# Performance work log

Measured on AMD Instinct MI355X. Metric: run time of the kernel, lower is better.

## Reference

```python
import jax, jax.numpy as jnp
import numpy as np

N_USERS = 200000
N_ITEMS = 100000
N_EDGES = 1000000
D = 64
NUM_LAYERS = 3
BATCH = 8192


def setup_inputs() -> dict:
    key = jax.random.key(0)
    ks = jax.random.split(key, 8)
    return {
        "user_feat": jax.random.normal(ks[0], (N_USERS, D), dtype=jnp.float32) * 0.1,
        "item_feat": jax.random.normal(ks[1], (N_ITEMS, D), dtype=jnp.float32) * 0.1,
        "edge_u": jax.random.randint(ks[2], (N_EDGES,), 0, N_USERS, dtype=jnp.int32),
        "edge_i": jax.random.randint(ks[3], (N_EDGES,), 0, N_ITEMS, dtype=jnp.int32),
        "norm": jax.random.uniform(ks[4], (N_EDGES,), dtype=jnp.float32),
        "users": jax.random.randint(ks[5], (BATCH,), 0, N_USERS, dtype=jnp.int32),
        "pos_items": jax.random.randint(ks[6], (BATCH,), 0, N_ITEMS, dtype=jnp.int32),
        "neg_items": jax.random.randint(ks[7], (BATCH,), 0, N_ITEMS, dtype=jnp.int32),
    }


def reference(user_feat, item_feat, edge_u, edge_i, norm, users, pos_items, neg_items):
    # LightGCN propagation: each layer does edge-weighted gather-scatter
    # (u_mul_e 'h','norm' -> sum) in both directions of the bipartite graph.
    u_h, i_h = user_feat, item_feat
    u_acc, i_acc = u_h, i_h
    w = norm[:, None]  # [E, 1]
    for _ in range(NUM_LAYERS):
        # user -> item messages
        new_i = jax.ops.segment_sum(u_h[edge_u] * w, edge_i, num_segments=N_ITEMS)
        # item -> user messages
        new_u = jax.ops.segment_sum(i_h[edge_i] * w, edge_u, num_segments=N_USERS)
        u_h, i_h = new_u, new_i
        u_acc = u_acc + u_h
        i_acc = i_acc + i_h
    scale = 1.0 / (NUM_LAYERS + 1)
    u_acc = u_acc * scale
    i_acc = i_acc * scale
    return (u_acc[users], i_acc[pos_items], i_acc[neg_items])
```

## Files before the change

### kernel.cpp

```cpp
#include <hip/hip_runtime.h>


#define N_USERS 200000
#define N_ITEMS 100000
#define N_EDGES 1000000
#define DIM 64
#define BATCH 8192
#define NTOT (N_USERS + N_ITEMS)
#define NOUT (3 * BATCH)
#define NPART 293
#define PLOCAL 1024
#define CAP 11264

#define HA 489
#define NUNITS (NTOT * DIM / 8)
#define OB (NOUT * 8 / 256)
#define AB8 (NTOT / 32)
#define PRB (NOUT / 1024)
#define PHB (NOUT * 8 / 1024)
#define CVB ((NUNITS + 4095) / 4096)
#define CPB ((NTOT / 4 + 1023) / 1024)

__device__ __forceinline__ unsigned f2bf(float f) {
    unsigned u = __float_as_uint(f);
    return (u + 0x7fffu + ((u >> 16) & 1u)) >> 16;
}
__device__ __forceinline__ uint2 pack4(float4 v) {
    uint2 o;
    o.x = f2bf(v.x) | (f2bf(v.y) << 16);
    o.y = f2bf(v.z) | (f2bf(v.w) << 16);
    return o;
}
__device__ __forceinline__ void fma4(float4& a, uint2 v, float w) {
    a.x += __uint_as_float(v.x << 16) * w;
    a.y += __uint_as_float(v.x & 0xffff0000u) * w;
    a.z += __uint_as_float(v.y << 16) * w;
    a.w += __uint_as_float(v.y & 0xffff0000u) * w;
}
__device__ __forceinline__ int out_bucket(int orow, const int* users,
                                          const int* pos, const int* neg) {
    int seg = orow >> 13;
    int b = orow & (BATCH - 1);
    if (seg == 0) return users[b];
    if (seg == 1) return N_USERS + pos[b];
    return N_USERS + neg[b];
}

__global__ void __launch_bounds__(1024)
prep_kernel(const int* __restrict__ users,
            const int* __restrict__ pos,
            const int* __restrict__ neg,
            const float* __restrict__ u_feat,
            const float* __restrict__ i_feat,
            unsigned char* __restrict__ isOut,
            int* __restrict__ flags,
            float* __restrict__ out)
{
    int bid = blockIdx.x, t = threadIdx.x;
    if (bid < PRB) {
        int orow = bid * 1024 + t;
        int bucket = out_bucket(orow, users, pos, neg);
        isOut[bucket] = 1;
        flags[bucket] = 1;
    } else {
        int idx = (bid - PRB) * 1024 + t;
        int row = idx >> 3;
        int d8 = (idx & 7) << 3;
        int seg = row >> 13;
        int b = row & (BATCH - 1);
        const float* src;
        if (seg == 0)      src = u_feat + (size_t)users[b] * DIM;
        else if (seg == 1) src = i_feat + (size_t)pos[b]   * DIM;
        else               src = i_feat + (size_t)neg[b]   * DIM;
        float4 v0 = *reinterpret_cast<const float4*>(src + d8);
        float4 v1 = *reinterpret_cast<const float4*>(src + d8 + 4);
        v0.x *= 0.25f; v0.y *= 0.25f; v0.z *= 0.25f; v0.w *= 0.25f;
        v1.x *= 0.25f; v1.y *= 0.25f; v1.z *= 0.25f; v1.w *= 0.25f;
        float* op = out + (size_t)row * DIM + d8;
        *reinterpret_cast<float4*>(op) = v0;
        *reinterpret_cast<float4*>(op + 4) = v1;
    }
}

__global__ void scatter_kernel(const int* __restrict__ eu,
                               const int* __restrict__ ei,
                               const float* __restrict__ w,
                               int* __restrict__ gcur,
                               uint2* __restrict__ partBuf,
                               const unsigned char* __restrict__ isOut,
                               int* __restrict__ flags)
{
    __shared__ int lh[NPART];
    __shared__ int lcur[NPART];
    int bid = blockIdx.x, t = threadIdx.x;
    for (int k = t; k < NPART; k += 256) lh[k] = 0;
    __syncthreads();
    int e0 = (bid * 256 + t) * 8;
    bool act = e0 < N_EDGES;
    int4 u0, u1, i0, i1;
    if (act) {
        u0 = *reinterpret_cast<const int4*>(eu + e0);
        u1 = *reinterpret_cast<const int4*>(eu + e0 + 4);
        i0 = *reinterpret_cast<const int4*>(ei + e0);
        i1 = *reinterpret_cast<const int4*>(ei + e0 + 4);
        atomicAdd(&lh[u0.x >> 10], 1);
        atomicAdd(&lh[u0.y >> 10], 1);
        atomicAdd(&lh[u0.z >> 10], 1);
        atomicAdd(&lh[u0.w >> 10], 1);
        atomicAdd(&lh[u1.x >> 10], 1);
        atomicAdd(&lh[u1.y >> 10], 1);
        atomicAdd(&lh[u1.z >> 10], 1);
        atomicAdd(&lh[u1.w >> 10], 1);
        atomicAdd(&lh[(N_USERS + i0.x) >> 10], 1);
        atomicAdd(&lh[(N_USERS + i0.y) >> 10], 1);
        atomicAdd(&lh[(N_USERS + i0.z) >> 10], 1);
        atomicAdd(&lh[(N_USERS + i0.w) >> 10], 1);
        atomicAdd(&lh[(N_USERS + i1.x) >> 10], 1);
        atomicAdd(&lh[(N_USERS + i1.y) >> 10], 1);
        atomicAdd(&lh[(N_USERS + i1.z) >> 10], 1);
        atomicAdd(&lh[(N_USERS + i1.w) >> 10], 1);
    }
    __syncthreads();
    for (int k = t; k < NPART; k += 256) {
        int v = lh[k];
        lcur[k] = v ? atomicAdd(&gcur[k], v) : 0;
    }
    __syncthreads();
    if (act) {
        float4 wa = *reinterpret_cast<const float4*>(w + e0);
        float4 wb = *reinterpret_cast<const float4*>(w + e0 + 4);
        int us[8] = {u0.x, u0.y, u0.z, u0.w, u1.x, u1.y, u1.z, u1.w};
        int is[8] = {i0.x, i0.y, i0.z, i0.w, i1.x, i1.y, i1.z, i1.w};
        float ws[8] = {wa.x, wa.y, wa.z, wa.w, wb.x, wb.y, wb.z, wb.w};
        #pragma unroll
        for (int j = 0; j < 8; ++j) {
            int bu = us[j];
            int bi = N_USERS + is[j];
            unsigned wbits = __float_as_uint(ws[j]);
            int pu = bu >> 10, pi = bi >> 10;
            int su = atomicAdd(&lcur[pu], 1);
            partBuf[(size_t)pu * CAP + su] =
                make_uint2((unsigned)(bu & 1023) | ((unsigned)bi << 10), wbits);
            int si = atomicAdd(&lcur[pi], 1);
            partBuf[(size_t)pi * CAP + si] =
                make_uint2((unsigned)(bi & 1023) | ((unsigned)bu << 10), wbits);
            if (isOut[bu]) flags[bi] = 1;
            if (isOut[bi]) flags[bu] = 1;
        }
    }
}

__global__ void __launch_bounds__(1024)
mid_kernel(const int* __restrict__ gcur,
           const uint2* __restrict__ partBuf,
           int2* __restrict__ rp2,
           int2* __restrict__ entries,
           const float4* __restrict__ uf4,
           const float4* __restrict__ if4,
           unsigned short* __restrict__ F0,
           const int* __restrict__ flags,
           int* __restrict__ list,
           int* __restrict__ count)
{
    __shared__ int h[PLOCAL];
    __shared__ int s[PLOCAL];
    __shared__ int cur[PLOCAL];
    int bid = blockIdx.x, t = threadIdx.x;
    if (bid < NPART) {
        int p = bid;
        int base = p * CAP;
        int end = base + gcur[p];
        h[t] = 0;
        __syncthreads();
        for (int r = base + t; r < end; r += 1024)
            atomicAdd(&h[partBuf[r].x & 1023], 1);
        __syncthreads();
        s[t] = h[t];
        __syncthreads();
        for (int off = 1; off < 1024; off <<= 1) {
            int x = (t >= off) ? s[t - off] : 0;
            __syncthreads();
            s[t] += x;
            __syncthreads();
        }
        int c0 = base + s[t] - h[t];
        cur[t] = c0;
        int gb = p * PLOCAL + t;
        if (gb < NTOT) rp2[gb] = make_int2(c0, h[t]);
        __syncthreads();
        for (int r = base + t; r < end; r += 1024) {
            uint2 rec = partBuf[r];
            int slot = atomicAdd(&cur[rec.x & 1023], 1);
            entries[slot] = make_int2((int)(rec.x >> 10), (int)rec.y);
        }
    } else if (bid < NPART + CVB) {
        const int NU4 = N_USERS * DIM / 4;
        int jb = (bid - NPART) * 4096 + t;
        float4 a[4], b[4];
        #pragma unroll
        for (int c = 0; c < 4; ++c) {
            int j = jb + c * 1024;
            if (j < NUNITS) {
                int f4 = j * 2;
                if (f4 < NU4) { a[c] = uf4[f4];       b[c] = uf4[f4 + 1]; }
                else          { a[c] = if4[f4 - NU4]; b[c] = if4[f4 - NU4 + 1]; }
            }
        }
        #pragma unroll
        for (int c = 0; c < 4; ++c) {
            int j = jb + c * 1024;
            if (j < NUNITS) {
                uint2 pa = pack4(a[c]), pb = pack4(b[c]);
                *reinterpret_cast<uint4*>(F0 + (size_t)j * 8) =
                    make_uint4(pa.x, pa.y, pb.x, pb.y);
            }
        }
    } else {
        int idx = ((bid - NPART - CVB) * 1024 + t) * 4;
        if (idx >= NTOT) return;
        int4 f = *reinterpret_cast<const int4*>(flags + idx);
        int loc[4]; int k = 0;
        if (f.x) loc[k++] = idx;
        if (f.y) loc[k++] = idx + 1;
        if (f.z) loc[k++] = idx + 2;
        if (f.w) loc[k++] = idx + 3;
        if (k) {
            int base = atomicAdd(count, k);
            for (int m = 0; m < k; ++m) list[base + m] = loc[m];
        }
    }
}

__device__ __forceinline__ void agg_row8(int2 rc, int l8, int gb,
                                         const int2* __restrict__ entries,
                                         const unsigned short* __restrict__ src,
                                         float4& sL, float4& sH)
{
    int beg = rc.x, cnt = rc.y;
    float4 a0L = {0,0,0,0}, a0H = {0,0,0,0}, a1L = {0,0,0,0}, a1H = {0,0,0,0};
    for (int base = 0; base < cnt; base += 8) {
        int2 e = make_int2(0, 0);
        if (base + l8 < cnt) e = entries[beg + base + l8];
        int   c[8];
        float wv[8];
        #pragma unroll
        for (int k = 0; k < 8; ++k) {
            c[k]  = __shfl(e.x, gb + k);
            wv[k] = __int_as_float(__shfl(e.y, gb + k));
        }
        uint4 v[8];
        #pragma unroll
        for (int k = 0; k < 8; ++k)
            v[k] = *reinterpret_cast<const uint4*>(
                src + (size_t)c[k] * DIM + l8 * 8);
        #pragma unroll
        for (int k = 0; k < 8; ++k) {
            if (k & 1) {
                fma4(a1L, make_uint2(v[k].x, v[k].y), wv[k]);
                fma4(a1H, make_uint2(v[k].z, v[k].w), wv[k]);
            } else {
                fma4(a0L, make_uint2(v[k].x, v[k].y), wv[k]);
                fma4(a0H, make_uint2(v[k].z, v[k].w), wv[k]);
            }
        }
    }
    sL.x = a0L.x + a1L.x; sL.y = a0L.y + a1L.y;
    sL.z = a0L.z + a1L.z; sL.w = a0L.w + a1L.w;
    sH.x = a0H.x + a1H.x; sH.y = a0H.y + a1H.y;
    sH.z = a0H.z + a1H.z; sH.w = a0H.w + a1H.w;
}

__global__ void agg1_kernel(const int2* __restrict__ rp2,
                            const int2* __restrict__ entries,
                            const unsigned short* __restrict__ F0,
                            unsigned short* __restrict__ H1)
{
    int gid = blockIdx.x * 256 + threadIdx.x;
    int lane = gid & 63;
    int l8 = lane & 7;
    int gb = lane & 56;
    int row = gid >> 3;
    if (row >= NTOT) return;
    float4 sL, sH;
    agg_row8(rp2[row], l8, gb, entries, F0, sL, sH);
    uint2 pL = pack4(sL), pH = pack4(sH);
    *reinterpret_cast<uint4*>(H1 + (size_t)row * DIM + l8 * 8) =
        make_uint4(pL.x, pL.y, pH.x, pH.y);
}

__global__ void agg2_add1_kernel(const int2* __restrict__ rp2,
                                 const int2* __restrict__ entries,
                                 const unsigned short* __restrict__ H1,
                                 unsigned short* __restrict__ H2,
                                 const int* __restrict__ list,
                                 const int* __restrict__ count,
                                 const int* __restrict__ users,
                                 const int* __restrict__ pos,
                                 const int* __restrict__ neg,
                                 float* __restrict__ out)
{
    int bid = blockIdx.x;
    if (bid < AB8) {
        int gid = bid * 256 + threadIdx.x;
        int lane = gid & 63;
        int l8 = lane & 7;
        int gb = lane & 56;
        int idx = gid >> 3;
        int n = *count;
        if (idx >= n) return;
        int row = list[idx];
        float4 sL, sH;
        agg_row8(rp2[row], l8, gb, entries, H1, sL, sH);
        uint2 pL = pack4(sL), pH = pack4(sH);
        *reinterpret_cast<uint4*>(H2 + (size_t)row * DIM + l8 * 8) =
            make_uint4(pL.x, pL.y, pH.x, pH.y);
    } else {
        int idx = (bid - AB8) * 256 + threadIdx.x;
        int row = idx >> 3;
        if (row >= NOUT) return;
        int d8 = (idx & 7) << 3;
        int bucket = out_bucket(row, users, pos, neg);
        uint4 v = *reinterpret_cast<const uint4*>(H1 + (size_t)bucket * DIM + d8);
        float* op = out + (size_t)row * DIM + d8;
        float4 o0 = *reinterpret_cast<const float4*>(op);
        float4 o1 = *reinterpret_cast<const float4*>(op + 4);
        o0.x += 0.25f * __uint_as_float(v.x << 16);
        o0.y += 0.25f * __uint_as_float(v.x & 0xffff0000u);
        o0.z += 0.25f * __uint_as_float(v.y << 16);
        o0.w += 0.25f * __uint_as_float(v.y & 0xffff0000u);
        o1.x += 0.25f * __uint_as_float(v.z << 16);
        o1.y += 0.25f * __uint_as_float(v.z & 0xffff0000u);
        o1.z += 0.25f * __uint_as_float(v.w << 16);
        o1.w += 0.25f * __uint_as_float(v.w & 0xffff0000u);
        *reinterpret_cast<float4*>(op) = o0;
        *reinterpret_cast<float4*>(op + 4) = o1;
    }
}

__global__ void aggout_add2_kernel(const int2* __restrict__ rp2,
                                   const int2* __restrict__ entries,
                                   const unsigned short* __restrict__ H2,
                                   const int* __restrict__ users,
                                   const int* __restrict__ pos,
                                   const int* __restrict__ neg,
                                   float* __restrict__ out)
{
    int gid = blockIdx.x * 256 + threadIdx.x;
    int lane = gid & 63;
    int l8 = lane & 7;
    int gb = lane & 56;
    int orow = gid >> 3;
    if (orow >= NOUT) return;
    int bucket = out_bucket(orow, users, pos, neg);
    float4 sL, sH;
    agg_row8(rp2[bucket], l8, gb, entries, H2, sL, sH);
    uint4 v = *reinterpret_cast<const uint4*>(H2 + (size_t)bucket * DIM + l8 * 8);
    sL.x += __uint_as_float(v.x << 16);
    sL.y += __uint_as_float(v.x & 0xffff0000u);
    sL.z += __uint_as_float(v.y << 16);
    sL.w += __uint_as_float(v.y & 0xffff0000u);
    sH.x += __uint_as_float(v.z << 16);
    sH.y += __uint_as_float(v.z & 0xffff0000u);
    sH.z += __uint_as_float(v.w << 16);
    sH.w += __uint_as_float(v.w & 0xffff0000u);
    float* op = out + (size_t)orow * DIM + l8 * 8;
    float4 o0 = *reinterpret_cast<const float4*>(op);
    float4 o1 = *reinterpret_cast<const float4*>(op + 4);
    o0.x += 0.25f * sL.x; o0.y += 0.25f * sL.y;
    o0.z += 0.25f * sL.z; o0.w += 0.25f * sL.w;
    o1.x += 0.25f * sH.x; o1.y += 0.25f * sH.y;
    o1.z += 0.25f * sH.z; o1.w += 0.25f * sH.w;
    *reinterpret_cast<float4*>(op) = o0;
    *reinterpret_cast<float4*>(op + 4) = o1;
}

extern "C" void kernel_launch(void* const* d_in, const int* in_sizes, int n_in,
                              void* d_out, int out_size, void* d_ws, size_t ws_size,
                              hipStream_t stream)
{
    const float* user_feat = (const float*)d_in[0];
    const float* item_feat = (const float*)d_in[1];
    const int*   eu        = (const int*)d_in[2];
    const int*   ei        = (const int*)d_in[3];
    const float* norm      = (const float*)d_in[4];
    const int*   users     = (const int*)d_in[5];
    const int*   pos       = (const int*)d_in[6];
    const int*   neg       = (const int*)d_in[7];
    float* out = (float*)d_out;

    auto align256 = [](size_t x) { return (x + 255) & ~(size_t)255; };
    const size_t hBytes = (size_t)NTOT * DIM * sizeof(unsigned short);
    const size_t pBytes = (size_t)NPART * CAP * 8;

    char* p = (char*)d_ws;
    unsigned short* F0 = (unsigned short*)p; p += align256(hBytes);
    unsigned short* H1 = (unsigned short*)p; p += align256(hBytes);
    unsigned short* H2 = (unsigned short*)p; p += align256(hBytes);
    const size_t zBytes = (size_t)(512 + NTOT + 16) * 4 + NTOT;
    int* gcur = (int*)p;
    int* flags = gcur + 512;
    int* count = flags + NTOT;
    unsigned char* isOut = (unsigned char*)(count + 16);
    p += align256(zBytes);
    int2* rp2      = (int2*)p;  p += align256((size_t)NTOT * 8);
    uint2* partBuf = (uint2*)p; p += align256(pBytes);
    int*  list     = (int*)p;   p += align256((size_t)NTOT * 4);
    int2* entries  = (int2*)p;  p += align256(pBytes);

    hipMemsetAsync(gcur, 0, zBytes, stream);

    prep_kernel<<<PRB + PHB, 1024, 0, stream>>>(
        users, pos, neg, user_feat, item_feat, isOut, flags, out);

    scatter_kernel<<<HA, 256, 0, stream>>>(
        eu, ei, norm, gcur, partBuf, isOut, flags);

    mid_kernel<<<NPART + CVB + CPB, 1024, 0, stream>>>(
        gcur, partBuf, rp2, entries,
        (const float4*)user_feat, (const float4*)item_feat, F0,
        flags, list, count);

    agg1_kernel<<<AB8, 256, 0, stream>>>(rp2, entries, F0, H1);

    agg2_add1_kernel<<<AB8 + OB, 256, 0, stream>>>(
        rp2, entries, H1, H2, list, count, users, pos, neg, out);

    aggout_add2_kernel<<<NOUT / 32, 256, 0, stream>>>(
        rp2, entries, H2, users, pos, neg, out);
}
```

Before: 267.2 us.

## Co-schedule bf16 conversion with edge scatter; shrink CSR build blocks to 256

```diff
diff --git a/kernel.cpp b/kernel.cpp
--- a/kernel.cpp
+++ b/kernel.cpp
@@ -14,12 +14,12 @@
 
 #define HA 489
 #define NUNITS (NTOT * DIM / 8)
+#define CB ((NUNITS + 1023) / 1024)
 #define OB (NOUT * 8 / 256)
 #define AB8 (NTOT / 32)
 #define PRB (NOUT / 1024)
 #define PHB (NOUT * 8 / 1024)
-#define CVB ((NUNITS + 4095) / 4096)
-#define CPB ((NTOT / 4 + 1023) / 1024)
+#define CPB ((NTOT / 4 + 255) / 256)
 
 __device__ __forceinline__ unsigned f2bf(float f) {
     unsigned u = __float_as_uint(f);
@@ -82,124 +82,84 @@
     }
 }
 
-__global__ void scatter_kernel(const int* __restrict__ eu,
-                               const int* __restrict__ ei,
-                               const float* __restrict__ w,
-                               int* __restrict__ gcur,
-                               uint2* __restrict__ partBuf,
-                               const unsigned char* __restrict__ isOut,
-                               int* __restrict__ flags)
-{
-    __shared__ int lh[NPART];
-    __shared__ int lcur[NPART];
+__global__ void __launch_bounds__(256)
+front_kernel(const int* __restrict__ eu,
+             const int* __restrict__ ei,
+             const float* __restrict__ w,
+             int* __restrict__ gcur,
+             uint2* __restrict__ partBuf,
+             const unsigned char* __restrict__ isOut,
+             int* __restrict__ flags,
+             const float4* __restrict__ uf4,
+             const float4* __restrict__ if4,
+             unsigned short* __restrict__ F0)
+{
     int bid = blockIdx.x, t = threadIdx.x;
-    for (int k = t; k < NPART; k += 256) lh[k] = 0;
-    __syncthreads();
-    int e0 = (bid * 256 + t) * 8;
-    bool act = e0 < N_EDGES;
-    int4 u0, u1, i0, i1;
-    if (act) {
-        u0 = *reinterpret_cast<const int4*>(eu + e0);
-        u1 = *reinterpret_cast<const int4*>(eu + e0 + 4);
-        i0 = *reinterpret_cast<const int4*>(ei + e0);
-        i1 = *reinterpret_cast<const int4*>(ei + e0 + 4);
-        atomicAdd(&lh[u0.x >> 10], 1);
-        atomicAdd(&lh[u0.y >> 10], 1);
-        atomicAdd(&lh[u0.z >> 10], 1);
-        atomicAdd(&lh[u0.w >> 10], 1);
-        atomicAdd(&lh[u1.x >> 10], 1);
-        atomicAdd(&lh[u1.y >> 10], 1);
-        atomicAdd(&lh[u1.z >> 10], 1);
-        atomicAdd(&lh[u1.w >> 10], 1);
-        atomicAdd(&lh[(N_USERS + i0.x) >> 10], 1);
-        atomicAdd(&lh[(N_USERS + i0.y) >> 10], 1);
-        atomicAdd(&lh[(N_USERS + i0.z) >> 10], 1);
-        atomicAdd(&lh[(N_USERS + i0.w) >> 10], 1);
-        atomicAdd(&lh[(N_USERS + i1.x) >> 10], 1);
-        atomicAdd(&lh[(N_USERS + i1.y) >> 10], 1);
-        atomicAdd(&lh[(N_USERS + i1.z) >> 10], 1);
-        atomicAdd(&lh[(N_USERS + i1.w) >> 10], 1);
-    }
-    __syncthreads();
-    for (int k = t; k < NPART; k += 256) {
-        int v = lh[k];
-        lcur[k] = v ? atomicAdd(&gcur[k], v) : 0;
-    }
-    __syncthreads();
-    if (act) {
-        float4 wa = *reinterpret_cast<const float4*>(w + e0);
-        float4 wb = *reinterpret_cast<const float4*>(w + e0 + 4);
-        int us[8] = {u0.x, u0.y, u0.z, u0.w, u1.x, u1.y, u1.z, u1.w};
-        int is[8] = {i0.x, i0.y, i0.z, i0.w, i1.x, i1.y, i1.z, i1.w};
-        float ws[8] = {wa.x, wa.y, wa.z, wa.w, wb.x, wb.y, wb.z, wb.w};
-        #pragma unroll
-        for (int j = 0; j < 8; ++j) {
-            int bu = us[j];
-            int bi = N_USERS + is[j];
-            unsigned wbits = __float_as_uint(ws[j]);
-            int pu = bu >> 10, pi = bi >> 10;
-            int su = atomicAdd(&lcur[pu], 1);
-            partBuf[(size_t)pu * CAP + su] =
-                make_uint2((unsigned)(bu & 1023) | ((unsigned)bi << 10), wbits);
-            int si = atomicAdd(&lcur[pi], 1);
-            partBuf[(size_t)pi * CAP + si] =
-                make_uint2((unsigned)(bi & 1023) | ((unsigned)bu << 10), wbits);
-            if (isOut[bu]) flags[bi] = 1;
-            if (isOut[bi]) flags[bu] = 1;
-        }
-    }
-}
-
-__global__ void __launch_bounds__(1024)
-mid_kernel(const int* __restrict__ gcur,
-           const uint2* __restrict__ partBuf,
-           int2* __restrict__ rp2,
-           int2* __restrict__ entries,
-           const float4* __restrict__ uf4,
-           const float4* __restrict__ if4,
-           unsigned short* __restrict__ F0,
-           const int* __restrict__ flags,
-           int* __restrict__ list,
-           int* __restrict__ count)
-{
-    __shared__ int h[PLOCAL];
-    __shared__ int s[PLOCAL];
-    __shared__ int cur[PLOCAL];
-    int bid = blockIdx.x, t = threadIdx.x;
-    if (bid < NPART) {
-        int p = bid;
-        int base = p * CAP;
-        int end = base + gcur[p];
-        h[t] = 0;
-        __syncthreads();
-        for (int r = base + t; r < end; r += 1024)
-            atomicAdd(&h[partBuf[r].x & 1023], 1);
-        __syncthreads();
-        s[t] = h[t];
-        __syncthreads();
-        for (int off = 1; off < 1024; off <<= 1) {
-            int x = (t >= off) ? s[t - off] : 0;
-            __syncthreads();
-            s[t] += x;
-            __syncthreads();
-        }
-        int c0 = base + s[t] - h[t];
-        cur[t] = c0;
-        int gb = p * PLOCAL + t;
-        if (gb < NTOT) rp2[gb] = make_int2(c0, h[t]);
-        __syncthreads();
-        for (int r = base + t; r < end; r += 1024) {
-            uint2 rec = partBuf[r];
-            int slot = atomicAdd(&cur[rec.x & 1023], 1);
-            entries[slot] = make_int2((int)(rec.x >> 10), (int)rec.y);
-        }
-    } else if (bid < NPART + CVB) {
+    if (bid < HA) {
+        __shared__ int lh[NPART];
+        __shared__ int lcur[NPART];
+        for (int k = t; k < NPART; k += 256) lh[k] = 0;
+        __syncthreads();
+        int e0 = (bid * 256 + t) * 8;
+        bool act = e0 < N_EDGES;
+        int4 u0, u1, i0, i1;
+        if (act) {
+            u0 = *reinterpret_cast<const int4*>(eu + e0);
+            u1 = *reinterpret_cast<const int4*>(eu + e0 + 4);
+            i0 = *reinterpret_cast<const int4*>(ei + e0);
+            i1 = *reinterpret_cast<const int4*>(ei + e0 + 4);
+            atomicAdd(&lh[u0.x >> 10], 1);
+            atomicAdd(&lh[u0.y >> 10], 1);
+            atomicAdd(&lh[u0.z >> 10], 1);
+            atomicAdd(&lh[u0.w >> 10], 1);
+            atomicAdd(&lh[u1.x >> 10], 1);
+            atomicAdd(&lh[u1.y >> 10], 1);
+            atomicAdd(&lh[u1.z >> 10], 1);
+            atomicAdd(&lh[u1.w >> 10], 1);
+            atomicAdd(&lh[(N_USERS + i0.x) >> 10], 1);
+            atomicAdd(&lh[(N_USERS + i0.y) >> 10], 1);
+            atomicAdd(&lh[(N_USERS + i0.z) >> 10], 1);
+            atomicAdd(&lh[(N_USERS + i0.w) >> 10], 1);
+            atomicAdd(&lh[(N_USERS + i1.x) >> 10], 1);
+            atomicAdd(&lh[(N_USERS + i1.y) >> 10], 1);
+            atomicAdd(&lh[(N_USERS + i1.z) >> 10], 1);
+            atomicAdd(&lh[(N_USERS + i1.w) >> 10], 1);
+        }
+        __syncthreads();
+        for (int k = t; k < NPART; k += 256) {
+            int v = lh[k];
+            lcur[k] = v ? atomicAdd(&gcur[k], v) : 0;
+        }
+        __syncthreads();
+        if (act) {
+            float4 wa = *reinterpret_cast<const float4*>(w + e0);
+            float4 wb = *reinterpret_cast<const float4*>(w + e0 + 4);
+            int us[8] = {u0.x, u0.y, u0.z, u0.w, u1.x, u1.y, u1.z, u1.w};
+            int is[8] = {i0.x, i0.y, i0.z, i0.w, i1.x, i1.y, i1.z, i1.w};
+            float ws[8] = {wa.x, wa.y, wa.z, wa.w, wb.x, wb.y, wb.z, wb.w};
+            #pragma unroll
+            for (int j = 0; j < 8; ++j) {
+                int bu = us[j];
+                int bi = N_USERS + is[j];
+                unsigned wbits = __float_as_uint(ws[j]);
+                int pu = bu >> 10, pi = bi >> 10;
+                int su = atomicAdd(&lcur[pu], 1);
+                partBuf[(size_t)pu * CAP + su] =
+                    make_uint2((unsigned)(bu & 1023) | ((unsigned)bi << 10), wbits);
+                int si = atomicAdd(&lcur[pi], 1);
+                partBuf[(size_t)pi * CAP + si] =
+                    make_uint2((unsigned)(bi & 1023) | ((unsigned)bu << 10), wbits);
+                if (isOut[bu]) flags[bi] = 1;
+                if (isOut[bi]) flags[bu] = 1;
+            }
+        }
+    } else {
         const int NU4 = N_USERS * DIM / 4;
-        int jb = (bid - NPART) * 4096 + t;
+        int jb = (bid - HA) * 1024 + t;
         float4 a[4], b[4];
         #pragma unroll
         for (int c = 0; c < 4; ++c) {
-            int j = jb + c * 1024;
+            int j = jb + c * 256;
             if (j < NUNITS) {
                 int f4 = j * 2;
                 if (f4 < NU4) { a[c] = uf4[f4];       b[c] = uf4[f4 + 1]; }
@@ -208,15 +168,65 @@
         }
         #pragma unroll
         for (int c = 0; c < 4; ++c) {
-            int j = jb + c * 1024;
+            int j = jb + c * 256;
             if (j < NUNITS) {
                 uint2 pa = pack4(a[c]), pb = pack4(b[c]);
                 *reinterpret_cast<uint4*>(F0 + (size_t)j * 8) =
                     make_uint4(pa.x, pa.y, pb.x, pb.y);
             }
         }
+    }
+}
+
+__global__ void __launch_bounds__(256)
+csr_compact_kernel(const int* __restrict__ gcur,
+                   const uint2* __restrict__ partBuf,
+                   int2* __restrict__ rp2,
+                   int2* __restrict__ entries,
+                   const int* __restrict__ flags,
+                   int* __restrict__ list,
+                   int* __restrict__ count)
+{
+    int bid = blockIdx.x, t = threadIdx.x;
+    if (bid < NPART) {
+        __shared__ int h[PLOCAL];
+        __shared__ int s[256];
+        __shared__ int cur[PLOCAL];
+        int p = bid;
+        int base = p * CAP;
+        int end = base + gcur[p];
+        h[t * 4 + 0] = 0; h[t * 4 + 1] = 0; h[t * 4 + 2] = 0; h[t * 4 + 3] = 0;
+        __syncthreads();
+        for (int r = base + t; r < end; r += 256)
+            atomicAdd(&h[partBuf[r].x & 1023], 1);
+        __syncthreads();
+        int h0 = h[t * 4], h1 = h[t * 4 + 1], h2 = h[t * 4 + 2], h3 = h[t * 4 + 3];
+        s[t] = h0 + h1 + h2 + h3;
+        __syncthreads();
+        for (int off = 1; off < 256; off <<= 1) {
+            int x = (t >= off) ? s[t - off] : 0;
+            __syncthreads();
+            s[t] += x;
+            __syncthreads();
+        }
+        int b0 = base + ((t == 0) ? 0 : s[t - 1]);
+        cur[t * 4 + 0] = b0;
+        cur[t * 4 + 1] = b0 + h0;
+        cur[t * 4 + 2] = b0 + h0 + h1;
+        cur[t * 4 + 3] = b0 + h0 + h1 + h2;
+        int hv[4] = {h0, h1, h2, h3};
+        int gb = p * PLOCAL + t * 4;
+        #pragma unroll
+        for (int k = 0; k < 4; ++k)
+            if (gb + k < NTOT) rp2[gb + k] = make_int2(cur[t * 4 + k], hv[k]);
+        __syncthreads();
+        for (int r = base + t; r < end; r += 256) {
+            uint2 rec = partBuf[r];
+            int slot = atomicAdd(&cur[rec.x & 1023], 1);
+            entries[slot] = make_int2((int)(rec.x >> 10), (int)rec.y);
+        }
     } else {
-        int idx = ((bid - NPART - CVB) * 1024 + t) * 4;
+        int idx = ((bid - NPART) * 256 + t) * 4;
         if (idx >= NTOT) return;
         int4 f = *reinterpret_cast<const int4*>(flags + idx);
         int loc[4]; int k = 0;
@@ -412,13 +422,12 @@
     prep_kernel<<<PRB + PHB, 1024, 0, stream>>>(
         users, pos, neg, user_feat, item_feat, isOut, flags, out);
 
-    scatter_kernel<<<HA, 256, 0, stream>>>(
-        eu, ei, norm, gcur, partBuf, isOut, flags);
-
-    mid_kernel<<<NPART + CVB + CPB, 1024, 0, stream>>>(
-        gcur, partBuf, rp2, entries,
-        (const float4*)user_feat, (const float4*)item_feat, F0,
-        flags, list, count);
+    front_kernel<<<HA + CB, 256, 0, stream>>>(
+        eu, ei, norm, gcur, partBuf, isOut, flags,
+        (const float4*)user_feat, (const float4*)item_feat, F0);
+
+    csr_compact_kernel<<<NPART + CPB, 256, 0, stream>>>(
+        gcur, partBuf, rp2, entries, flags, list, count);
 
     agg1_kernel<<<AB8, 256, 0, stream>>>(rp2, entries, F0, H1);
 
```

Result: slower. 293.0 us (+9.7%).

## Move bf16 feature conversion into scatter kernel and use nontemporal accesses

Applied to the files above, without the earlier changes.

```diff
diff --git a/kernel.cpp b/kernel.cpp
--- a/kernel.cpp
+++ b/kernel.cpp
@@ -14,12 +14,15 @@
 
 #define HA 489
 #define NUNITS (NTOT * DIM / 8)
+#define CB ((NUNITS + 1023) / 1024)
 #define OB (NOUT * 8 / 256)
 #define AB8 (NTOT / 32)
 #define PRB (NOUT / 1024)
 #define PHB (NOUT * 8 / 1024)
-#define CVB ((NUNITS + 4095) / 4096)
 #define CPB ((NTOT / 4 + 1023) / 1024)
+
+typedef float    floatx4 __attribute__((ext_vector_type(4)));
+typedef unsigned uint4v  __attribute__((ext_vector_type(4)));
 
 __device__ __forceinline__ unsigned f2bf(float f) {
     unsigned u = __float_as_uint(f);
@@ -29,6 +32,12 @@
     uint2 o;
     o.x = f2bf(v.x) | (f2bf(v.y) << 16);
     o.y = f2bf(v.z) | (f2bf(v.w) << 16);
+    return o;
+}
+__device__ __forceinline__ uint2 pack4v(floatx4 v) {
+    uint2 o;
+    o.x = f2bf(v[0]) | (f2bf(v[1]) << 16);
+    o.y = f2bf(v[2]) | (f2bf(v[3]) << 16);
     return o;
 }
 __device__ __forceinline__ void fma4(float4& a, uint2 v, float w) {
@@ -82,91 +91,121 @@
     }
 }
 
-__global__ void scatter_kernel(const int* __restrict__ eu,
-                               const int* __restrict__ ei,
-                               const float* __restrict__ w,
-                               int* __restrict__ gcur,
-                               uint2* __restrict__ partBuf,
-                               const unsigned char* __restrict__ isOut,
-                               int* __restrict__ flags)
-{
-    __shared__ int lh[NPART];
-    __shared__ int lcur[NPART];
+__global__ void __launch_bounds__(256)
+front_kernel(const int* __restrict__ eu,
+             const int* __restrict__ ei,
+             const float* __restrict__ w,
+             int* __restrict__ gcur,
+             uint2* __restrict__ partBuf,
+             const unsigned char* __restrict__ isOut,
+             int* __restrict__ flags,
+             const floatx4* __restrict__ uf4,
+             const floatx4* __restrict__ if4,
+             unsigned short* __restrict__ F0)
+{
     int bid = blockIdx.x, t = threadIdx.x;
-    for (int k = t; k < NPART; k += 256) lh[k] = 0;
-    __syncthreads();
-    int e0 = (bid * 256 + t) * 8;
-    bool act = e0 < N_EDGES;
-    int4 u0, u1, i0, i1;
-    if (act) {
-        u0 = *reinterpret_cast<const int4*>(eu + e0);
-        u1 = *reinterpret_cast<const int4*>(eu + e0 + 4);
-        i0 = *reinterpret_cast<const int4*>(ei + e0);
-        i1 = *reinterpret_cast<const int4*>(ei + e0 + 4);
-        atomicAdd(&lh[u0.x >> 10], 1);
-        atomicAdd(&lh[u0.y >> 10], 1);
-        atomicAdd(&lh[u0.z >> 10], 1);
-        atomicAdd(&lh[u0.w >> 10], 1);
-        atomicAdd(&lh[u1.x >> 10], 1);
-        atomicAdd(&lh[u1.y >> 10], 1);
-        atomicAdd(&lh[u1.z >> 10], 1);
-        atomicAdd(&lh[u1.w >> 10], 1);
-        atomicAdd(&lh[(N_USERS + i0.x) >> 10], 1);
-        atomicAdd(&lh[(N_USERS + i0.y) >> 10], 1);
-        atomicAdd(&lh[(N_USERS + i0.z) >> 10], 1);
-        atomicAdd(&lh[(N_USERS + i0.w) >> 10], 1);
-        atomicAdd(&lh[(N_USERS + i1.x) >> 10], 1);
-        atomicAdd(&lh[(N_USERS + i1.y) >> 10], 1);
-        atomicAdd(&lh[(N_USERS + i1.z) >> 10], 1);
-        atomicAdd(&lh[(N_USERS + i1.w) >> 10], 1);
+    if (bid < HA) {
+        __shared__ int lh[NPART];
+        __shared__ int lcur[NPART];
+        for (int k = t; k < NPART; k += 256) lh[k] = 0;
+        __syncthreads();
+        int e0 = (bid * 256 + t) * 8;
+        bool act = e0 < N_EDGES;
+        int4 u0, u1, i0, i1;
+        if (act) {
+            u0 = *reinterpret_cast<const int4*>(eu + e0);
+            u1 = *reinterpret_cast<const int4*>(eu + e0 + 4);
+            i0 = *reinterpret_cast<const int4*>(ei + e0);
+            i1 = *reinterpret_cast<const int4*>(ei + e0 + 4);
+            atomicAdd(&lh[u0.x >> 10], 1);
+            atomicAdd(&lh[u0.y >> 10], 1);
+            atomicAdd(&lh[u0.z >> 10], 1);
+            atomicAdd(&lh[u0.w >> 10], 1);
+            atomicAdd(&lh[u1.x >> 10], 1);
+            atomicAdd(&lh[u1.y >> 10], 1);
+            atomicAdd(&lh[u1.z >> 10], 1);
+            atomicAdd(&lh[u1.w >> 10], 1);
+            atomicAdd(&lh[(N_USERS + i0.x) >> 10], 1);
+            atomicAdd(&lh[(N_USERS + i0.y) >> 10], 1);
+            atomicAdd(&lh[(N_USERS + i0.z) >> 10], 1);
+            atomicAdd(&lh[(N_USERS + i0.w) >> 10], 1);
+            atomicAdd(&lh[(N_USERS + i1.x) >> 10], 1);
+            atomicAdd(&lh[(N_USERS + i1.y) >> 10], 1);
+            atomicAdd(&lh[(N_USERS + i1.z) >> 10], 1);
+            atomicAdd(&lh[(N_USERS + i1.w) >> 10], 1);
+        }
+        __syncthreads();
+        for (int k = t; k < NPART; k += 256) {
+            int v = lh[k];
+            lcur[k] = v ? atomicAdd(&gcur[k], v) : 0;
+        }
+        __syncthreads();
+        if (act) {
+            float4 wa = *reinterpret_cast<const float4*>(w + e0);
+            float4 wb = *reinterpret_cast<const float4*>(w + e0 + 4);
+            int us[8] = {u0.x, u0.y, u0.z, u0.w, u1.x, u1.y, u1.z, u1.w};
+            int is[8] = {i0.x, i0.y, i0.z, i0.w, i1.x, i1.y, i1.z, i1.w};
+            float ws[8] = {wa.x, wa.y, wa.z, wa.w, wb.x, wb.y, wb.z, wb.w};
+            #pragma unroll
+            for (int j = 0; j < 8; ++j) {
+                int bu = us[j];
+                int bi = N_USERS + is[j];
+                unsigned wbits = __float_as_uint(ws[j]);
+                int pu = bu >> 10, pi = bi >> 10;
+                int su = atomicAdd(&lcur[pu], 1);
+                partBuf[(size_t)pu * CAP + su] =
+                    make_uint2((unsigned)(bu & 1023) | ((unsigned)bi << 10), wbits);
+                int si = atomicAdd(&lcur[pi], 1);
+                partBuf[(size_t)pi * CAP + si] =
+                    make_uint2((unsigned)(bi & 1023) | ((unsigned)bu << 10), wbits);
+                if (isOut[bu]) flags[bi] = 1;
+                if (isOut[bi]) flags[bu] = 1;
+            }
+        }
+    } else {
+        const int NU4 = N_USERS * DIM / 4;
+        int jb = (bid - HA) * 1024 + t;
+        floatx4 a[4], b[4];
+        #pragma unroll
+        for (int c = 0; c < 4; ++c) {
+            int j = jb + c * 256;
+            if (j < NUNITS) {
+                int f4 = j * 2;
+                if (f4 < NU4) {
+                    a[c] = __builtin_nontemporal_load(uf4 + f4);
+                    b[c] = __builtin_nontemporal_load(uf4 + f4 + 1);
+                } else {
+                    a[c] = __builtin_nontemporal_load(if4 + (f4 - NU4));
+                    b[c] = __builtin_nontemporal_load(if4 + (f4 - NU4) + 1);
+                }
+            }
+        }
+        #pragma unroll
+        for (int c = 0; c < 4; ++c) {
+            int j = jb + c * 256;
+            if (j < NUNITS) {
+                uint2 pa = pack4v(a[c]), pb = pack4v(b[c]);
+                uint4v o = {pa.x, pa.y, pb.x, pb.y};
+                __builtin_nontemporal_store(o, (uint4v*)(F0 + (size_t)j * 8));
+            }
+        }
     }
-    __syncthreads();
-    for (int k = t; k < NPART; k += 256) {
-        int v = lh[k];
-        lcur[k] = v ? atomicAdd(&gcur[k], v) : 0;
-    }
-    __syncthreads();
-    if (act) {
-        float4 wa = *reinterpret_cast<const float4*>(w + e0);
-        float4 wb = *reinterpret_cast<const float4*>(w + e0 + 4);
-        int us[8] = {u0.x, u0.y, u0.z, u0.w, u1.x, u1.y, u1.z, u1.w};
-        int is[8] = {i0.x, i0.y, i0.z, i0.w, i1.x, i1.y, i1.z, i1.w};
-        float ws[8] = {wa.x, wa.y, wa.z, wa.w, wb.x, wb.y, wb.z, wb.w};
-        #pragma unroll
-        for (int j = 0; j < 8; ++j) {
-            int bu = us[j];
-            int bi = N_USERS + is[j];
-            unsigned wbits = __float_as_uint(ws[j]);
-            int pu = bu >> 10, pi = bi >> 10;
-            int su = atomicAdd(&lcur[pu], 1);
-            partBuf[(size_t)pu * CAP + su] =
-                make_uint2((unsigned)(bu & 1023) | ((unsigned)bi << 10), wbits);
-            int si = atomicAdd(&lcur[pi], 1);
-            partBuf[(size_t)pi * CAP + si] =
-                make_uint2((unsigned)(bi & 1023) | ((unsigned)bu << 10), wbits);
-            if (isOut[bu]) flags[bi] = 1;
-            if (isOut[bi]) flags[bu] = 1;
-        }
-    }
 }
 
 __global__ void __launch_bounds__(1024)
-mid_kernel(const int* __restrict__ gcur,
-           const uint2* __restrict__ partBuf,
-           int2* __restrict__ rp2,
-           int2* __restrict__ entries,
-           const float4* __restrict__ uf4,
-           const float4* __restrict__ if4,
-           unsigned short* __restrict__ F0,
-           const int* __restrict__ flags,
-           int* __restrict__ list,
-           int* __restrict__ count)
-{
-    __shared__ int h[PLOCAL];
-    __shared__ int s[PLOCAL];
-    __shared__ int cur[PLOCAL];
+csr_compact_kernel(const int* __restrict__ gcur,
+                   const uint2* __restrict__ partBuf,
+                   int2* __restrict__ rp2,
+                   int2* __restrict__ entries,
+                   const int* __restrict__ flags,
+                   int* __restrict__ list,
+                   int* __restrict__ count)
+{
     int bid = blockIdx.x, t = threadIdx.x;
     if (bid < NPART) {
+        __shared__ int h[PLOCAL];
+        __shared__ int s[PLOCAL];
+        __shared__ int cur[PLOCAL];
         int p = bid;
         int base = p * CAP;
         int end = base + gcur[p];
@@ -193,30 +232,8 @@
             int slot = atomicAdd(&cur[rec.x & 1023], 1);
             entries[slot] = make_int2((int)(rec.x >> 10), (int)rec.y);
         }
-    } else if (bid < NPART + CVB) {
-        const int NU4 = N_USERS * DIM / 4;
-        int jb = (bid - NPART) * 4096 + t;
-        float4 a[4], b[4];
-        #pragma unroll
-        for (int c = 0; c < 4; ++c) {
-            int j = jb + c * 1024;
-            if (j < NUNITS) {
-                int f4 = j * 2;
-                if (f4 < NU4) { a[c] = uf4[f4];       b[c] = uf4[f4 + 1]; }
-                else          { a[c] = if4[f4 - NU4]; b[c] = if4[f4 - NU4 + 1]; }
-            }
-        }
-        #pragma unroll
-        for (int c = 0; c < 4; ++c) {
-            int j = jb + c * 1024;
-            if (j < NUNITS) {
-                uint2 pa = pack4(a[c]), pb = pack4(b[c]);
-                *reinterpret_cast<uint4*>(F0 + (size_t)j * 8) =
-                    make_uint4(pa.x, pa.y, pb.x, pb.y);
-            }
-        }
     } else {
-        int idx = ((bid - NPART - CVB) * 1024 + t) * 4;
+        int idx = ((bid - NPART) * 1024 + t) * 4;
         if (idx >= NTOT) return;
         int4 f = *reinterpret_cast<const int4*>(flags + idx);
         int loc[4]; int k = 0;
@@ -412,13 +429,12 @@
     prep_kernel<<<PRB + PHB, 1024, 0, stream>>>(
         users, pos, neg, user_feat, item_feat, isOut, flags, out);
 
-    scatter_kernel<<<HA, 256, 0, stream>>>(
-        eu, ei, norm, gcur, partBuf, isOut, flags);
-
-    mid_kernel<<<NPART + CVB + CPB, 1024, 0, stream>>>(
-        gcur, partBuf, rp2, entries,
-        (const float4*)user_feat, (const float4*)item_feat, F0,
-        flags, list, count);
+    front_kernel<<<HA + CB, 256, 0, stream>>>(
+        eu, ei, norm, gcur, partBuf, isOut, flags,
+        (const floatx4*)user_feat, (const floatx4*)item_feat, F0);
+
+    csr_compact_kernel<<<NPART + CPB, 1024, 0, stream>>>(
+        gcur, partBuf, rp2, entries, flags, list, count);
 
     agg1_kernel<<<AB8, 256, 0, stream>>>(rp2, entries, F0, H1);
 
```

New measurement: 295.6 us. 1.11x slower.
